# Performance work log

Hardware: AMD Instinct MI355X
Metric: run time of the kernel (lower is better)

Reference implementation:

```python
import jax, jax.numpy as jnp
import numpy as np

N, E, H, D, IN = 50000, 800000, 4, 64, 2  # nodes, edges, heads, head_dim, in_dim
NEG_SLOPE = 0.2  # DGL GATConv default leaky_relu slope


def setup_inputs() -> dict:
    key = jax.random.key(0)
    ks = jax.random.split(key, 16)
    p = lambda k, shape: jax.random.normal(k, shape, jnp.float32) * 0.1
    return dict(
        positions=jax.random.normal(ks[0], (N, IN), jnp.float32),
        src=jax.random.randint(ks[1], (E,), 0, N, jnp.int32),
        dst=jax.random.randint(ks[2], (E,), 0, N, jnp.int32),
        # conv1: in=2 -> 4 heads x 64; residual needs a projection (2 != 256)
        W1=p(ks[3], (IN, H * D)), al1=p(ks[4], (H, D)), ar1=p(ks[5], (H, D)),
        resW1=p(ks[6], (IN, H * D)),
        # conv2/conv3: in=256 == H*D -> identity residual in DGL
        W2=p(ks[7], (H * D, H * D)), al2=p(ks[8], (H, D)), ar2=p(ks[9], (H, D)),
        W3=p(ks[10], (H * D, H * D)), al3=p(ks[11], (H, D)), ar3=p(ks[12], (H, D)),
        # edge-scoring MLP: Linear(64,64)+ReLU, Linear(64,1)+Sigmoid
        mW1=p(ks[13], (D, D)), mb1=jnp.zeros((D,), jnp.float32),
        mW2=p(ks[14], (D, 1)), mb2=jnp.zeros((1,), jnp.float32),
    )


def _gat_layer(h, W, al, ar, src, dst, res, activation):
    """One DGL-style GATConv. h:[N,Fin] -> [N,H,D]. res:[N,H,D] residual."""
    feat = (h @ W).reshape(N, H, D)
    el = (feat * al).sum(-1)                       # [N,H]
    er = (feat * ar).sum(-1)                       # [N,H]
    e = jax.nn.leaky_relu(el[src] + er[dst], NEG_SLOPE)  # [E,H]
    # edge softmax over incoming edges of each dst node
    emax = jax.ops.segment_max(e, dst, num_segments=N)
    emax = jnp.where(jnp.isfinite(emax), emax, 0.0)      # guard empty segments
    ex = jnp.exp(e - emax[dst])
    den = jax.ops.segment_sum(ex, dst, num_segments=N)
    alpha = ex / jnp.maximum(den, 1e-9)[dst]             # [E,H]
    out = jax.ops.segment_sum(feat[src] * alpha[:, :, None], dst, num_segments=N)
    out = out + res
    if activation:
        out = jax.nn.relu(out)
    return out


def reference(positions, W1, al1, ar1, resW1, W2, al2, ar2, W3, al3, ar3,
              mW1, mb1, mW2, mb2, src, dst):
    res1 = (positions @ resW1).reshape(N, H, D)
    h = _gat_layer(positions, W1, al1, ar1, src, dst, res1, True).reshape(N, H * D)
    h = _gat_layer(h, W2, al2, ar2, src, dst, h.reshape(N, H, D), True).reshape(N, H * D)
    h = _gat_layer(h, W3, al3, ar3, src, dst, h.reshape(N, H, D), False).mean(1)  # [N,D]
    x = jnp.abs(h[src] - h[dst])                   # [E,D]
    score = jax.nn.sigmoid(jax.nn.relu(x @ mW1 + mb1) @ mW2 + mb2)
    return score.squeeze(-1)                       # [E]
```

## Files before the change

kernel.cpp:

```cpp
#include <hip/hip_runtime.h>
#include <hip/hip_bf16.h>

#define NN 50000
#define EE 800000

typedef short short8 __attribute__((ext_vector_type(8)));
typedef float f32x4 __attribute__((ext_vector_type(4)));

__device__ __forceinline__ float lrelu(float x) { return x > 0.f ? x : 0.2f * x; }

__device__ __forceinline__ unsigned short f2bf(float x) {
    __hip_bfloat16 b = __float2bfloat16(x);
    return *(unsigned short*)&b;
}
__device__ __forceinline__ float bf2f(unsigned short u) {
    return __uint_as_float(((unsigned int)u) << 16);
}

__global__ void hist_k(const int* __restrict__ dst, int* __restrict__ deg) {
    int i = blockIdx.x * 256 + threadIdx.x;
    if (i < EE) atomicAdd(&deg[dst[i]], 1);
}

__global__ __launch_bounds__(1024) void scan_k(const int* __restrict__ deg,
                                               int* __restrict__ row_ptr,
                                               int* __restrict__ cursor) {
    __shared__ int wsum[16];
    int tid = threadIdx.x, lane = tid & 63, w = tid >> 6;
    int carry = 0;
    for (int base = 0; base < NN; base += 1024) {
        int i = base + tid;
        int v = (i < NN) ? deg[i] : 0;
        int x = v;
#pragma unroll
        for (int off = 1; off < 64; off <<= 1) {
            int y = __shfl_up(x, off);
            if (lane >= off) x += y;
        }
        if (lane == 63) wsum[w] = x;
        __syncthreads();
        if (tid < 16) {
            int s = wsum[tid];
#pragma unroll
            for (int off = 1; off < 16; off <<= 1) {
                int y = __shfl_up(s, off);
                if (tid >= off) s += y;
            }
            wsum[tid] = s;
        }
        __syncthreads();
        int woff = w ? wsum[w - 1] : 0;
        int excl = carry + woff + x - v;
        if (i < NN) { row_ptr[i] = excl; cursor[i] = excl; }
        carry += wsum[15];
        __syncthreads();
    }
    if (tid == 0) row_ptr[NN] = carry;
}

__global__ void scatter_k(const int* __restrict__ src, const int* __restrict__ dst,
                          int* __restrict__ cursor, int* __restrict__ csr_src) {
    int i = blockIdx.x * 256 + threadIdx.x;
    if (i < EE) {
        int slot = atomicAdd(&cursor[dst[i]], 1);
        csr_src[slot] = src[i];
    }
}

__global__ __launch_bounds__(256) void bconv_k(const float* __restrict__ W2,
                                               const float* __restrict__ W3,
                                               const float* __restrict__ mW1,
                                               unsigned short* __restrict__ BT2,
                                               unsigned short* __restrict__ BT3,
                                               unsigned short* __restrict__ W1Tb) {
    int tid = blockIdx.x * 256 + threadIdx.x;
    int k = tid & 255, n = tid >> 8;
    BT2[n * 256 + k] = f2bf(W2[k * 256 + n]);
    BT3[n * 256 + k] = f2bf(W3[k * 256 + n]);
    if (tid < 4096) {
        int kk = tid & 63, nn = tid >> 6;
        W1Tb[nn * 64 + kk] = f2bf(mW1[kk * 64 + nn]);
    }
}

__global__ __launch_bounds__(256) void eler1_k(const float* __restrict__ pos,
                                               const float* __restrict__ W1,
                                               const float* __restrict__ al,
                                               const float* __restrict__ ar,
                                               float* __restrict__ el,
                                               float* __restrict__ er) {
    int wid = blockIdx.x * 4 + (threadIdx.x >> 6);
    int lane = threadIdx.x & 63;
    if (wid >= NN) return;
    int f = lane * 4;
    float4 w0 = *(const float4*)&W1[f];
    float4 w1 = *(const float4*)&W1[256 + f];
    float4 a4 = *(const float4*)&al[f];
    float4 r4 = *(const float4*)&ar[f];
    float2 p = *(const float2*)&pos[wid * 2];
    float fx = p.x * w0.x + p.y * w1.x;
    float fy = p.x * w0.y + p.y * w1.y;
    float fz = p.x * w0.z + p.y * w1.z;
    float fw = p.x * w0.w + p.y * w1.w;
    float pl = fx * a4.x + fy * a4.y + fz * a4.z + fw * a4.w;
    float pr = fx * r4.x + fy * r4.y + fz * r4.z + fw * r4.w;
#pragma unroll
    for (int off = 1; off < 16; off <<= 1) {
        pl += __shfl_xor(pl, off);
        pr += __shfl_xor(pr, off);
    }
    if ((lane & 15) == 0) {
        int h = lane >> 4;
        el[wid * 4 + h] = pl;
        er[wid * 4 + h] = pr;
    }
}

__global__ __launch_bounds__(256) void agg1_k(const float* __restrict__ pos,
                                              const float* __restrict__ W1,
                                              const float* __restrict__ resW1,
                                              const float* __restrict__ el,
                                              const float* __restrict__ er,
                                              const int* __restrict__ row_ptr,
                                              const int* __restrict__ csr_src,
                                              unsigned short* __restrict__ hb16) {
    int wid = blockIdx.x * 4 + (threadIdx.x >> 6);
    int lane = threadIdx.x & 63;
    if (wid >= NN) return;
    int f = lane * 4;
    int start = row_ptr[wid], end = row_ptr[wid + 1];
    int h = lane >> 4;
    float eh = er[wid * 4 + h];

    float ap0 = 0.f, ap1 = 0.f, den = 0.f;
    int s = start;
    for (; s + 3 < end; s += 4) {
        int sn0 = csr_src[s], sn1 = csr_src[s + 1];
        int sn2 = csr_src[s + 2], sn3 = csr_src[s + 3];
        float e0 = el[sn0 * 4 + h], e1 = el[sn1 * 4 + h];
        float e2 = el[sn2 * 4 + h], e3 = el[sn3 * 4 + h];
        float2 p0 = *(const float2*)&pos[sn0 * 2];
        float2 p1 = *(const float2*)&pos[sn1 * 2];
        float2 p2 = *(const float2*)&pos[sn2 * 2];
        float2 p3 = *(const float2*)&pos[sn3 * 2];
        float w0 = __expf(lrelu(e0 + eh)), w1 = __expf(lrelu(e1 + eh));
        float w2 = __expf(lrelu(e2 + eh)), w3 = __expf(lrelu(e3 + eh));
        den += (w0 + w1) + (w2 + w3);
        ap0 += w0 * p0.x + w1 * p1.x + w2 * p2.x + w3 * p3.x;
        ap1 += w0 * p0.y + w1 * p1.y + w2 * p2.y + w3 * p3.y;
    }
    for (; s < end; ++s) {
        int sn = csr_src[s];
        float w = __expf(lrelu(el[sn * 4 + h] + eh));
        float2 p = *(const float2*)&pos[sn * 2];
        den += w;
        ap0 += w * p.x;
        ap1 += w * p.y;
    }
    float inv = 1.f / fmaxf(den, 1e-9f);
    ap0 *= inv;
    ap1 *= inv;

    float4 w0 = *(const float4*)&W1[f];
    float4 w1 = *(const float4*)&W1[256 + f];
    float4 rw0 = *(const float4*)&resW1[f];
    float4 rw1 = *(const float4*)&resW1[256 + f];
    float2 pd = *(const float2*)&pos[wid * 2];
    float4 o;
    o.x = fmaxf(ap0 * w0.x + ap1 * w1.x + pd.x * rw0.x + pd.y * rw1.x, 0.f);
    o.y = fmaxf(ap0 * w0.y + ap1 * w1.y + pd.x * rw0.y + pd.y * rw1.y, 0.f);
    o.z = fmaxf(ap0 * w0.z + ap1 * w1.z + pd.x * rw0.z + pd.y * rw1.z, 0.f);
    o.w = fmaxf(ap0 * w0.w + ap1 * w1.w + pd.x * rw0.w + pd.y * rw1.w, 0.f);
    ushort4 ob;
    ob.x = f2bf(o.x); ob.y = f2bf(o.y); ob.z = f2bf(o.z); ob.w = f2bf(o.w);
    *(ushort4*)&hb16[(size_t)wid * 256 + f] = ob;
}

__global__ __launch_bounds__(256) void agg_k(const unsigned short* __restrict__ featb,
                                             const float* __restrict__ el,
                                             const float* __restrict__ er,
                                             const int* __restrict__ row_ptr,
                                             const int* __restrict__ csr_src,
                                             unsigned short* __restrict__ hb16) {
    int wid = blockIdx.x * 4 + (threadIdx.x >> 6);
    int lane = threadIdx.x & 63;
    if (wid >= NN) return;
    int f = lane * 4;
    int start = row_ptr[wid], end = row_ptr[wid + 1];
    int h = lane >> 4;
    float eh = er[wid * 4 + h];

    float4 acc = {0.f, 0.f, 0.f, 0.f};
    float den = 0.f;
    int s = start;
    for (; s + 3 < end; s += 4) {
        int sn0 = csr_src[s], sn1 = csr_src[s + 1];
        int sn2 = csr_src[s + 2], sn3 = csr_src[s + 3];
        float e0 = el[sn0 * 4 + h], e1 = el[sn1 * 4 + h];
        float e2 = el[sn2 * 4 + h], e3 = el[sn3 * 4 + h];
        ushort4 v0 = *(const ushort4*)&featb[(size_t)sn0 * 256 + f];
        ushort4 v1 = *(const ushort4*)&featb[(size_t)sn1 * 256 + f];
        ushort4 v2 = *(const ushort4*)&featb[(size_t)sn2 * 256 + f];
        ushort4 v3 = *(const ushort4*)&featb[(size_t)sn3 * 256 + f];
        float w0 = __expf(lrelu(e0 + eh)), w1 = __expf(lrelu(e1 + eh));
        float w2 = __expf(lrelu(e2 + eh)), w3 = __expf(lrelu(e3 + eh));
        den += (w0 + w1) + (w2 + w3);
        acc.x += w0 * bf2f(v0.x) + w1 * bf2f(v1.x) + w2 * bf2f(v2.x) + w3 * bf2f(v3.x);
        acc.y += w0 * bf2f(v0.y) + w1 * bf2f(v1.y) + w2 * bf2f(v2.y) + w3 * bf2f(v3.y);
        acc.z += w0 * bf2f(v0.z) + w1 * bf2f(v1.z) + w2 * bf2f(v2.z) + w3 * bf2f(v3.z);
        acc.w += w0 * bf2f(v0.w) + w1 * bf2f(v1.w) + w2 * bf2f(v2.w) + w3 * bf2f(v3.w);
    }
    for (; s < end; ++s) {
        int sn = csr_src[s];
        float w = __expf(lrelu(el[sn * 4 + h] + eh));
        ushort4 v = *(const ushort4*)&featb[(size_t)sn * 256 + f];
        den += w;
        acc.x += w * bf2f(v.x);
        acc.y += w * bf2f(v.y);
        acc.z += w * bf2f(v.z);
        acc.w += w * bf2f(v.w);
    }
    float inv = 1.f / fmaxf(den, 1e-9f);
    ushort4 rb = *(const ushort4*)&hb16[(size_t)wid * 256 + f];
    float4 o;
    o.x = fmaxf(acc.x * inv + bf2f(rb.x), 0.f);
    o.y = fmaxf(acc.y * inv + bf2f(rb.y), 0.f);
    o.z = fmaxf(acc.z * inv + bf2f(rb.z), 0.f);
    o.w = fmaxf(acc.w * inv + bf2f(rb.w), 0.f);
    ushort4 ob;
    ob.x = f2bf(o.x); ob.y = f2bf(o.y); ob.z = f2bf(o.z); ob.w = f2bf(o.w);
    *(ushort4*)&hb16[(size_t)wid * 256 + f] = ob;
}

__global__ __launch_bounds__(256) void agg3_k(const unsigned short* __restrict__ featb,
                                              const float* __restrict__ el,
                                              const float* __restrict__ er,
                                              const int* __restrict__ row_ptr,
                                              const int* __restrict__ csr_src,
                                              const unsigned short* __restrict__ hresb,
                                              unsigned short* __restrict__ hsmallb) {
    int wid = blockIdx.x * 4 + (threadIdx.x >> 6);
    int lane = threadIdx.x & 63;
    if (wid >= NN) return;
    int f = lane * 4;
    int start = row_ptr[wid], end = row_ptr[wid + 1];
    int h = lane >> 4;
    float eh = er[wid * 4 + h];

    float4 acc = {0.f, 0.f, 0.f, 0.f};
    float den = 0.f;
    int s = start;
    for (; s + 3 < end; s += 4) {
        int sn0 = csr_src[s], sn1 = csr_src[s + 1];
        int sn2 = csr_src[s + 2], sn3 = csr_src[s + 3];
        float e0 = el[sn0 * 4 + h], e1 = el[sn1 * 4 + h];
        float e2 = el[sn2 * 4 + h], e3 = el[sn3 * 4 + h];
        ushort4 v0 = *(const ushort4*)&featb[(size_t)sn0 * 256 + f];
        ushort4 v1 = *(const ushort4*)&featb[(size_t)sn1 * 256 + f];
        ushort4 v2 = *(const ushort4*)&featb[(size_t)sn2 * 256 + f];
        ushort4 v3 = *(const ushort4*)&featb[(size_t)sn3 * 256 + f];
        float w0 = __expf(lrelu(e0 + eh)), w1 = __expf(lrelu(e1 + eh));
        float w2 = __expf(lrelu(e2 + eh)), w3 = __expf(lrelu(e3 + eh));
        den += (w0 + w1) + (w2 + w3);
        acc.x += w0 * bf2f(v0.x) + w1 * bf2f(v1.x) + w2 * bf2f(v2.x) + w3 * bf2f(v3.x);
        acc.y += w0 * bf2f(v0.y) + w1 * bf2f(v1.y) + w2 * bf2f(v2.y) + w3 * bf2f(v3.y);
        acc.z += w0 * bf2f(v0.z) + w1 * bf2f(v1.z) + w2 * bf2f(v2.z) + w3 * bf2f(v3.z);
        acc.w += w0 * bf2f(v0.w) + w1 * bf2f(v1.w) + w2 * bf2f(v2.w) + w3 * bf2f(v3.w);
    }
    for (; s < end; ++s) {
        int sn = csr_src[s];
        float w = __expf(lrelu(el[sn * 4 + h] + eh));
        ushort4 v = *(const ushort4*)&featb[(size_t)sn * 256 + f];
        den += w;
        acc.x += w * bf2f(v.x);
        acc.y += w * bf2f(v.y);
        acc.z += w * bf2f(v.z);
        acc.w += w * bf2f(v.w);
    }
    float inv = 1.f / fmaxf(den, 1e-9f);
    ushort4 rb = *(const ushort4*)&hresb[(size_t)wid * 256 + f];
    float4 o;
    o.x = acc.x * inv + bf2f(rb.x);
    o.y = acc.y * inv + bf2f(rb.y);
    o.z = acc.z * inv + bf2f(rb.z);
    o.w = acc.w * inv + bf2f(rb.w);
    o.x += __shfl_xor(o.x, 16); o.y += __shfl_xor(o.y, 16);
    o.z += __shfl_xor(o.z, 16); o.w += __shfl_xor(o.w, 16);
    o.x += __shfl_xor(o.x, 32); o.y += __shfl_xor(o.y, 32);
    o.z += __shfl_xor(o.z, 32); o.w += __shfl_xor(o.w, 32);
    if (lane < 16) {
        ushort4 m4;
        m4.x = f2bf(o.x * 0.25f);
        m4.y = f2bf(o.y * 0.25f);
        m4.z = f2bf(o.z * 0.25f);
        m4.w = f2bf(o.w * 0.25f);
        *(ushort4*)&hsmallb[(size_t)wid * 64 + lane * 4] = m4;
    }
}

__global__ __launch_bounds__(256) void gemm_mfma_k(const unsigned short* __restrict__ Ab,
                                                   const unsigned short* __restrict__ BT,
                                                   const float* __restrict__ al,
                                                   const float* __restrict__ ar,
                                                   unsigned short* __restrict__ C,
                                                   float* __restrict__ el,
                                                   float* __restrict__ er) {
    __shared__ __align__(16) short As[128 * 40];
    __shared__ __align__(16) short Bs[128 * 40];
    int tid = threadIdx.x;
    int lane = tid & 63, wave = tid >> 6;
    int wr = wave >> 1, wc = wave & 1;
    int tileM = blockIdx.x * 128;
    int tileN = blockIdx.y * 128;

    int srow = tid >> 1, sko = (tid & 1) * 16;
    int fm = lane & 15, kg = lane >> 4;

    f32x4 acc[4][4];
#pragma unroll
    for (int i = 0; i < 4; ++i)
#pragma unroll
        for (int j = 0; j < 4; ++j) acc[i][j] = (f32x4){0.f, 0.f, 0.f, 0.f};

    for (int k0 = 0; k0 < 256; k0 += 32) {
        int gr = tileM + srow;
        short8 a0 = (short8)0, a1 = (short8)0;
        if (gr < NN) {
            a0 = *(const short8*)&Ab[(size_t)gr * 256 + k0 + sko];
            a1 = *(const short8*)&Ab[(size_t)gr * 256 + k0 + sko + 8];
        }
        *(short8*)&As[srow * 40 + sko] = a0;
        *(short8*)&As[srow * 40 + sko + 8] = a1;
        short8 b0 = *(const short8*)&BT[(size_t)(tileN + srow) * 256 + k0 + sko];
        short8 b1 = *(const short8*)&BT[(size_t)(tileN + srow) * 256 + k0 + sko + 8];
        *(short8*)&Bs[srow * 40 + sko] = b0;
        *(short8*)&Bs[srow * 40 + sko + 8] = b1;
        __syncthreads();

        short8 afr[4], bfr[4];
#pragma unroll
        for (int mi = 0; mi < 4; ++mi)
            afr[mi] = *(const short8*)&As[(wr * 64 + mi * 16 + fm) * 40 + kg * 8];
#pragma unroll
        for (int ni = 0; ni < 4; ++ni)
            bfr[ni] = *(const short8*)&Bs[(wc * 64 + ni * 16 + fm) * 40 + kg * 8];
#pragma unroll
        for (int mi = 0; mi < 4; ++mi)
#pragma unroll
            for (int ni = 0; ni < 4; ++ni)
                acc[mi][ni] = __builtin_amdgcn_mfma_f32_16x16x32_bf16(
                    afr[mi], bfr[ni], acc[mi][ni], 0, 0, 0);
        __syncthreads();
    }

#pragma unroll
    for (int mi = 0; mi < 4; ++mi) {
#pragma unroll
        for (int ni = 0; ni < 4; ++ni) {
            int col = tileN + wc * 64 + ni * 16 + fm;
#pragma unroll
            for (int r = 0; r < 4; ++r) {
                int row = tileM + wr * 64 + mi * 16 + kg * 4 + r;
                if (row < NN) C[(size_t)row * 256 + col] = f2bf(acc[mi][ni][r]);
            }
        }
    }

    int h = blockIdx.y * 2 + wc;
    float al_r[4], ar_r[4];
#pragma unroll
    for (int ni = 0; ni < 4; ++ni) {
        al_r[ni] = al[h * 64 + ni * 16 + fm];
        ar_r[ni] = ar[h * 64 + ni * 16 + fm];
    }
#pragma unroll
    for (int mi = 0; mi < 4; ++mi) {
#pragma unroll
        for (int r = 0; r < 4; ++r) {
            float tl = acc[mi][0][r] * al_r[0] + acc[mi][1][r] * al_r[1] +
                       acc[mi][2][r] * al_r[2] + acc[mi][3][r] * al_r[3];
            float tr = acc[mi][0][r] * ar_r[0] + acc[mi][1][r] * ar_r[1] +
                       acc[mi][2][r] * ar_r[2] + acc[mi][3][r] * ar_r[3];
#pragma unroll
            for (int off = 1; off < 16; off <<= 1) {
                tl += __shfl_xor(tl, off);
                tr += __shfl_xor(tr, off);
            }
            if (fm == 0) {
                int row = tileM + wr * 64 + mi * 16 + kg * 4 + r;
                if (row < NN) {
                    el[row * 4 + h] = tl;
                    er[row * 4 + h] = tr;
                }
            }
        }
    }
}

__global__ __launch_bounds__(256) void edge_score4_k(const unsigned short* __restrict__ hs,
                                                     const int* __restrict__ src,
                                                     const int* __restrict__ dst,
                                                     const unsigned short* __restrict__ W1Tb,
                                                     const float* __restrict__ mb1,
                                                     const float* __restrict__ mW2,
                                                     const float* __restrict__ mb2,
                                                     float* __restrict__ out) {
    __shared__ __align__(16) unsigned short xs[64 * 72];
    __shared__ __align__(16) unsigned short wt[64 * 72];
    __shared__ float b1s[64], w2s[64];
    int tid = threadIdx.x;
    int e_loc = tid >> 2, q = tid & 3;

    *(short8*)&wt[e_loc * 72 + q * 16]     = *(const short8*)&W1Tb[e_loc * 64 + q * 16];
    *(short8*)&wt[e_loc * 72 + q * 16 + 8] = *(const short8*)&W1Tb[e_loc * 64 + q * 16 + 8];
    if (tid < 64) { b1s[tid] = mb1[tid]; w2s[tid] = mW2[tid]; }

    int e = blockIdx.x * 64 + e_loc;
    int s = src[e], d = dst[e];
    const unsigned short* rs = &hs[(size_t)s * 64 + q * 16];
    const unsigned short* rd = &hs[(size_t)d * 64 + q * 16];
    short8 a0 = *(const short8*)&rs[0];
    short8 a1 = *(const short8*)&rs[8];
    short8 b0 = *(const short8*)&rd[0];
    short8 b1 = *(const short8*)&rd[8];
    short8 x0, x1;
#pragma unroll
    for (int i = 0; i < 8; ++i) {
        x0[i] = (short)f2bf(fabsf(bf2f((unsigned short)a0[i]) - bf2f((unsigned short)b0[i])));
        x1[i] = (short)f2bf(fabsf(bf2f((unsigned short)a1[i]) - bf2f((unsigned short)b1[i])));
    }
    *(short8*)&xs[e_loc * 72 + q * 16]     = x0;
    *(short8*)&xs[e_loc * 72 + q * 16 + 8] = x1;
    __syncthreads();

    int lane = tid & 63, w = tid >> 6;
    int fm = lane & 15, kg = lane >> 4;

    const unsigned short* arow = &xs[(w * 16 + fm) * 72];
    short8 af0 = *(const short8*)&arow[kg * 8];
    short8 af1 = *(const short8*)&arow[32 + kg * 8];

    f32x4 acc[4];
#pragma unroll
    for (int ni = 0; ni < 4; ++ni) acc[ni] = (f32x4){0.f, 0.f, 0.f, 0.f};
#pragma unroll
    for (int ni = 0; ni < 4; ++ni) {
        const unsigned short* brow = &wt[(ni * 16 + fm) * 72];
        short8 bf0 = *(const short8*)&brow[kg * 8];
        short8 bf1 = *(const short8*)&brow[32 + kg * 8];
        acc[ni] = __builtin_amdgcn_mfma_f32_16x16x32_bf16(af0, bf0, acc[ni], 0, 0, 0);
        acc[ni] = __builtin_amdgcn_mfma_f32_16x16x32_bf16(af1, bf1, acc[ni], 0, 0, 0);
    }

    float t0 = 0.f, t1 = 0.f, t2 = 0.f, t3 = 0.f;
#pragma unroll
    for (int ni = 0; ni < 4; ++ni) {
        int n = ni * 16 + fm;
        float bb = b1s[n], ww = w2s[n];
        t0 += fmaxf(acc[ni][0] + bb, 0.f) * ww;
        t1 += fmaxf(acc[ni][1] + bb, 0.f) * ww;
        t2 += fmaxf(acc[ni][2] + bb, 0.f) * ww;
        t3 += fmaxf(acc[ni][3] + bb, 0.f) * ww;
    }
#pragma unroll
    for (int off = 1; off < 16; off <<= 1) {
        t0 += __shfl_xor(t0, off);
        t1 += __shfl_xor(t1, off);
        t2 += __shfl_xor(t2, off);
        t3 += __shfl_xor(t3, off);
    }
    if (fm == 0) {
        float bias = mb2[0];
        int base = blockIdx.x * 64 + w * 16 + kg * 4;
        out[base + 0] = 1.f / (1.f + __expf(-(t0 + bias)));
        out[base + 1] = 1.f / (1.f + __expf(-(t1 + bias)));
        out[base + 2] = 1.f / (1.f + __expf(-(t2 + bias)));
        out[base + 3] = 1.f / (1.f + __expf(-(t3 + bias)));
    }
}

extern "C" void kernel_launch(void* const* d_in, const int* in_sizes, int n_in,
                              void* d_out, int out_size, void* d_ws, size_t ws_size,
                              hipStream_t stream) {
    (void)in_sizes; (void)n_in; (void)out_size; (void)ws_size;
    const float* pos   = (const float*)d_in[0];
    const int*   src   = (const int*)d_in[1];
    const int*   dst   = (const int*)d_in[2];
    const float* W1    = (const float*)d_in[3];
    const float* al1   = (const float*)d_in[4];
    const float* ar1   = (const float*)d_in[5];
    const float* resW1 = (const float*)d_in[6];
    const float* W2    = (const float*)d_in[7];
    const float* al2   = (const float*)d_in[8];
    const float* ar2   = (const float*)d_in[9];
    const float* W3    = (const float*)d_in[10];
    const float* al3   = (const float*)d_in[11];
    const float* ar3   = (const float*)d_in[12];
    const float* mW1   = (const float*)d_in[13];
    const float* mb1   = (const float*)d_in[14];
    const float* mW2   = (const float*)d_in[15];
    const float* mb2   = (const float*)d_in[16];
    float* out = (float*)d_out;

    char* ws = (char*)d_ws;
    size_t off = 0;
    auto alloc = [&](size_t bytes) {
        void* p = ws + off;
        off += (bytes + 255) & ~(size_t)255;
        return p;
    };
    unsigned short* FEATb  = (unsigned short*)alloc((size_t)NN * 256 * 2);
    unsigned short* Hb16   = (unsigned short*)alloc((size_t)NN * 256 * 2);
    unsigned short* BT2    = (unsigned short*)alloc((size_t)256 * 256 * 2);
    unsigned short* BT3    = (unsigned short*)alloc((size_t)256 * 256 * 2);
    unsigned short* W1Tb   = (unsigned short*)alloc((size_t)64 * 64 * 2);
    unsigned short* hsmallb = (unsigned short*)alloc((size_t)NN * 64 * 2);
    float* el     = (float*)alloc((size_t)NN * 4 * 4);
    float* er     = (float*)alloc((size_t)NN * 4 * 4);
    int* deg      = (int*)alloc((size_t)NN * 4);
    int* row_ptr  = (int*)alloc((size_t)(NN + 1) * 4);
    int* cursor   = (int*)alloc((size_t)NN * 4);
    int* csr      = (int*)alloc((size_t)EE * 4);

    hipMemsetAsync(deg, 0, (size_t)NN * 4, stream);
    hist_k<<<(EE + 255) / 256, 256, 0, stream>>>(dst, deg);
    scan_k<<<1, 1024, 0, stream>>>(deg, row_ptr, cursor);
    scatter_k<<<(EE + 255) / 256, 256, 0, stream>>>(src, dst, cursor, csr);
    bconv_k<<<256, 256, 0, stream>>>(W2, W3, mW1, BT2, BT3, W1Tb);

    eler1_k<<<NN / 4 + 1, 256, 0, stream>>>(pos, W1, al1, ar1, el, er);
    agg1_k<<<NN / 4 + 1, 256, 0, stream>>>(pos, W1, resW1, el, er, row_ptr, csr, Hb16);

    dim3 ggrid((NN + 127) / 128, 2);
    gemm_mfma_k<<<ggrid, 256, 0, stream>>>(Hb16, BT2, al2, ar2, FEATb, el, er);
    agg_k<<<NN / 4 + 1, 256, 0, stream>>>(FEATb, el, er, row_ptr, csr, Hb16);

    gemm_mfma_k<<<ggrid, 256, 0, stream>>>(Hb16, BT3, al3, ar3, FEATb, el, er);
    agg3_k<<<NN / 4 + 1, 256, 0, stream>>>(FEATb, el, er, row_ptr, csr, Hb16, hsmallb);

    edge_score4_k<<<EE / 64, 256, 0, stream>>>(hsmallb, src, dst, W1Tb, mb1, mW2, mb2, out);
}
```

Baseline: 494.0 us.

## Parallelize degree scan across blocks and unroll neighbor gathers by eight

Replaces the single-block serial prefix scan over 50000 node degrees with a three-kernel multi-block scan: per-block scan, a scan of block totals, then an offset fix-up. Separately, the edge-aggregation loops in all three GAT layers now issue eight neighbor index, score and feature loads before computing, instead of four. The scan change targets a long one-block serial kernel at the cost of two extra launches. The wider unroll aims to keep more memory requests in flight, at the cost of more registers and a longer scalar tail loop for low-degree nodes.

```diff
diff --git a/kernel.cpp b/kernel.cpp
--- a/kernel.cpp
+++ b/kernel.cpp
@@ -3,6 +3,7 @@
 
 #define NN 50000
 #define EE 800000
+#define NB 196
 
 typedef short short8 __attribute__((ext_vector_type(8)));
 typedef float f32x4 __attribute__((ext_vector_type(4)));
@@ -22,40 +23,64 @@
     if (i < EE) atomicAdd(&deg[dst[i]], 1);
 }
 
-__global__ __launch_bounds__(1024) void scan_k(const int* __restrict__ deg,
+__global__ __launch_bounds__(256) void scanA_k(const int* __restrict__ deg,
+                                               int* __restrict__ cscan,
+                                               int* __restrict__ bsum) {
+    __shared__ int wtot[4];
+    int tid = threadIdx.x, lane = tid & 63, w = tid >> 6;
+    int i = blockIdx.x * 256 + tid;
+    int v = (i < NN) ? deg[i] : 0;
+    int x = v;
+#pragma unroll
+    for (int off = 1; off < 64; off <<= 1) {
+        int y = __shfl_up(x, off);
+        if (lane >= off) x += y;
+    }
+    if (lane == 63) wtot[w] = x;
+    __syncthreads();
+    int prefix = 0;
+#pragma unroll
+    for (int j = 0; j < 4; ++j)
+        if (j < w) prefix += wtot[j];
+    x += prefix;
+    if (i < NN) cscan[i] = x;
+    if (tid == 255) bsum[blockIdx.x] = x;
+}
+
+__global__ __launch_bounds__(256) void scanB_k(const int* __restrict__ bsum,
+                                               int* __restrict__ boff) {
+    __shared__ int wtot[4];
+    int tid = threadIdx.x, lane = tid & 63, w = tid >> 6;
+    int v = (tid < NB) ? bsum[tid] : 0;
+    int x = v;
+#pragma unroll
+    for (int off = 1; off < 64; off <<= 1) {
+        int y = __shfl_up(x, off);
+        if (lane >= off) x += y;
+    }
+    if (lane == 63) wtot[w] = x;
+    __syncthreads();
+    int prefix = 0;
+#pragma unroll
+    for (int j = 0; j < 4; ++j)
+        if (j < w) prefix += wtot[j];
+    x += prefix;
+    if (tid < NB) boff[tid] = x - v;
+    if (tid == NB - 1) boff[NB] = x;
+}
+
+__global__ __launch_bounds__(256) void scanC_k(const int* __restrict__ deg,
+                                               const int* __restrict__ cscan,
+                                               const int* __restrict__ boff,
                                                int* __restrict__ row_ptr,
                                                int* __restrict__ cursor) {
-    __shared__ int wsum[16];
-    int tid = threadIdx.x, lane = tid & 63, w = tid >> 6;
-    int carry = 0;
-    for (int base = 0; base < NN; base += 1024) {
-        int i = base + tid;
-        int v = (i < NN) ? deg[i] : 0;
-        int x = v;
-#pragma unroll
-        for (int off = 1; off < 64; off <<= 1) {
-            int y = __shfl_up(x, off);
-            if (lane >= off) x += y;
-        }
-        if (lane == 63) wsum[w] = x;
-        __syncthreads();
-        if (tid < 16) {
-            int s = wsum[tid];
-#pragma unroll
-            for (int off = 1; off < 16; off <<= 1) {
-                int y = __shfl_up(s, off);
-                if (tid >= off) s += y;
-            }
-            wsum[tid] = s;
-        }
-        __syncthreads();
-        int woff = w ? wsum[w - 1] : 0;
-        int excl = carry + woff + x - v;
-        if (i < NN) { row_ptr[i] = excl; cursor[i] = excl; }
-        carry += wsum[15];
-        __syncthreads();
-    }
-    if (tid == 0) row_ptr[NN] = carry;
+    int i = blockIdx.x * 256 + threadIdx.x;
+    if (i < NN) {
+        int e = boff[i >> 8] + cscan[i] - deg[i];
+        row_ptr[i] = e;
+        cursor[i] = e;
+    }
+    if (i == 0) row_ptr[NN] = boff[NB];
 }
 
 __global__ void scatter_k(const int* __restrict__ src, const int* __restrict__ dst,
@@ -134,20 +159,24 @@
 
     float ap0 = 0.f, ap1 = 0.f, den = 0.f;
     int s = start;
-    for (; s + 3 < end; s += 4) {
-        int sn0 = csr_src[s], sn1 = csr_src[s + 1];
-        int sn2 = csr_src[s + 2], sn3 = csr_src[s + 3];
-        float e0 = el[sn0 * 4 + h], e1 = el[sn1 * 4 + h];
-        float e2 = el[sn2 * 4 + h], e3 = el[sn3 * 4 + h];
-        float2 p0 = *(const float2*)&pos[sn0 * 2];
-        float2 p1 = *(const float2*)&pos[sn1 * 2];
-        float2 p2 = *(const float2*)&pos[sn2 * 2];
-        float2 p3 = *(const float2*)&pos[sn3 * 2];
-        float w0 = __expf(lrelu(e0 + eh)), w1 = __expf(lrelu(e1 + eh));
-        float w2 = __expf(lrelu(e2 + eh)), w3 = __expf(lrelu(e3 + eh));
-        den += (w0 + w1) + (w2 + w3);
-        ap0 += w0 * p0.x + w1 * p1.x + w2 * p2.x + w3 * p3.x;
-        ap1 += w0 * p0.y + w1 * p1.y + w2 * p2.y + w3 * p3.y;
+    for (; s + 7 < end; s += 8) {
+        int sn[8];
+#pragma unroll
+        for (int j = 0; j < 8; ++j) sn[j] = csr_src[s + j];
+        float e[8];
+        float2 p[8];
+#pragma unroll
+        for (int j = 0; j < 8; ++j) {
+            e[j] = el[sn[j] * 4 + h];
+            p[j] = *(const float2*)&pos[sn[j] * 2];
+        }
+#pragma unroll
+        for (int j = 0; j < 8; ++j) {
+            float w = __expf(lrelu(e[j] + eh));
+            den += w;
+            ap0 += w * p[j].x;
+            ap1 += w * p[j].y;
+        }
     }
     for (; s < end; ++s) {
         int sn = csr_src[s];
@@ -193,22 +222,26 @@
     float4 acc = {0.f, 0.f, 0.f, 0.f};
     float den = 0.f;
     int s = start;
-    for (; s + 3 < end; s += 4) {
-        int sn0 = csr_src[s], sn1 = csr_src[s + 1];
-        int sn2 = csr_src[s + 2], sn3 = csr_src[s + 3];
-        float e0 = el[sn0 * 4 + h], e1 = el[sn1 * 4 + h];
-        float e2 = el[sn2 * 4 + h], e3 = el[sn3 * 4 + h];
-        ushort4 v0 = *(const ushort4*)&featb[(size_t)sn0 * 256 + f];
-        ushort4 v1 = *(const ushort4*)&featb[(size_t)sn1 * 256 + f];
-        ushort4 v2 = *(const ushort4*)&featb[(size_t)sn2 * 256 + f];
-        ushort4 v3 = *(const ushort4*)&featb[(size_t)sn3 * 256 + f];
-        float w0 = __expf(lrelu(e0 + eh)), w1 = __expf(lrelu(e1 + eh));
-        float w2 = __expf(lrelu(e2 + eh)), w3 = __expf(lrelu(e3 + eh));
-        den += (w0 + w1) + (w2 + w3);
-        acc.x += w0 * bf2f(v0.x) + w1 * bf2f(v1.x) + w2 * bf2f(v2.x) + w3 * bf2f(v3.x);
-        acc.y += w0 * bf2f(v0.y) + w1 * bf2f(v1.y) + w2 * bf2f(v2.y) + w3 * bf2f(v3.y);
-        acc.z += w0 * bf2f(v0.z) + w1 * bf2f(v1.z) + w2 * bf2f(v2.z) + w3 * bf2f(v3.z);
-        acc.w += w0 * bf2f(v0.w) + w1 * bf2f(v1.w) + w2 * bf2f(v2.w) + w3 * bf2f(v3.w);
+    for (; s + 7 < end; s += 8) {
+        int sn[8];
+#pragma unroll
+        for (int j = 0; j < 8; ++j) sn[j] = csr_src[s + j];
+        float e[8];
+        ushort4 v[8];
+#pragma unroll
+        for (int j = 0; j < 8; ++j) {
+            e[j] = el[sn[j] * 4 + h];
+            v[j] = *(const ushort4*)&featb[(size_t)sn[j] * 256 + f];
+        }
+#pragma unroll
+        for (int j = 0; j < 8; ++j) {
+            float w = __expf(lrelu(e[j] + eh));
+            den += w;
+            acc.x += w * bf2f(v[j].x);
+            acc.y += w * bf2f(v[j].y);
+            acc.z += w * bf2f(v[j].z);
+            acc.w += w * bf2f(v[j].w);
+        }
     }
     for (; s < end; ++s) {
         int sn = csr_src[s];
@@ -250,22 +283,26 @@
     float4 acc = {0.f, 0.f, 0.f, 0.f};
     float den = 0.f;
     int s = start;
-    for (; s + 3 < end; s += 4) {
-        int sn0 = csr_src[s], sn1 = csr_src[s + 1];
-        int sn2 = csr_src[s + 2], sn3 = csr_src[s + 3];
-        float e0 = el[sn0 * 4 + h], e1 = el[sn1 * 4 + h];
-        float e2 = el[sn2 * 4 + h], e3 = el[sn3 * 4 + h];
-        ushort4 v0 = *(const ushort4*)&featb[(size_t)sn0 * 256 + f];
-        ushort4 v1 = *(const ushort4*)&featb[(size_t)sn1 * 256 + f];
-        ushort4 v2 = *(const ushort4*)&featb[(size_t)sn2 * 256 + f];
-        ushort4 v3 = *(const ushort4*)&featb[(size_t)sn3 * 256 + f];
-        float w0 = __expf(lrelu(e0 + eh)), w1 = __expf(lrelu(e1 + eh));
-        float w2 = __expf(lrelu(e2 + eh)), w3 = __expf(lrelu(e3 + eh));
-        den += (w0 + w1) + (w2 + w3);
-        acc.x += w0 * bf2f(v0.x) + w1 * bf2f(v1.x) + w2 * bf2f(v2.x) + w3 * bf2f(v3.x);
-        acc.y += w0 * bf2f(v0.y) + w1 * bf2f(v1.y) + w2 * bf2f(v2.y) + w3 * bf2f(v3.y);
-        acc.z += w0 * bf2f(v0.z) + w1 * bf2f(v1.z) + w2 * bf2f(v2.z) + w3 * bf2f(v3.z);
-        acc.w += w0 * bf2f(v0.w) + w1 * bf2f(v1.w) + w2 * bf2f(v2.w) + w3 * bf2f(v3.w);
+    for (; s + 7 < end; s += 8) {
+        int sn[8];
+#pragma unroll
+        for (int j = 0; j < 8; ++j) sn[j] = csr_src[s + j];
+        float e[8];
+        ushort4 v[8];
+#pragma unroll
+        for (int j = 0; j < 8; ++j) {
+            e[j] = el[sn[j] * 4 + h];
+            v[j] = *(const ushort4*)&featb[(size_t)sn[j] * 256 + f];
+        }
+#pragma unroll
+        for (int j = 0; j < 8; ++j) {
+            float w = __expf(lrelu(e[j] + eh));
+            den += w;
+            acc.x += w * bf2f(v[j].x);
+            acc.y += w * bf2f(v[j].y);
+            acc.z += w * bf2f(v[j].z);
+            acc.w += w * bf2f(v[j].w);
+        }
     }
     for (; s < end; ++s) {
         int sn = csr_src[s];
@@ -518,13 +555,18 @@
     float* el     = (float*)alloc((size_t)NN * 4 * 4);
     float* er     = (float*)alloc((size_t)NN * 4 * 4);
     int* deg      = (int*)alloc((size_t)NN * 4);
+    int* cscan    = (int*)alloc((size_t)NN * 4);
+    int* bsum     = (int*)alloc((size_t)NB * 4);
+    int* boff     = (int*)alloc((size_t)(NB + 1) * 4);
     int* row_ptr  = (int*)alloc((size_t)(NN + 1) * 4);
     int* cursor   = (int*)alloc((size_t)NN * 4);
     int* csr      = (int*)alloc((size_t)EE * 4);
 
     hipMemsetAsync(deg, 0, (size_t)NN * 4, stream);
     hist_k<<<(EE + 255) / 256, 256, 0, stream>>>(dst, deg);
-    scan_k<<<1, 1024, 0, stream>>>(deg, row_ptr, cursor);
+    scanA_k<<<NB, 256, 0, stream>>>(deg, cscan, bsum);
+    scanB_k<<<1, 256, 0, stream>>>(bsum, boff);
+    scanC_k<<<NB, 256, 0, stream>>>(deg, cscan, boff, row_ptr, cursor);
     scatter_k<<<(EE + 255) / 256, 256, 0, stream>>>(src, dst, cursor, csr);
     bconv_k<<<256, 256, 0, stream>>>(W2, W3, mW1, BT2, BT3, W1Tb);
 
```

Measured after the change: 458.3 us. -7.2%, faster.

## Parallelize degree scan and drop LDS staging in GEMM and edge scorer

Applied to the files above, without the earlier changes.

Replaces the single-block serial prefix scan with a three-kernel multi-block scan (block scans, block-offset scan, fixup), removing a long single-workgroup loop. The bf16 MFMA GEMM now loads A/B fragments directly from global memory instead of staging through shared memory with barriers. The edge scorer likewise reads weights and biases directly from global memory instead of copying them to LDS. The changes trade LDS traffic and barriers for possibly less coalesced, repeated global reads, and add two extra kernel launches.

```diff
diff --git a/kernel.cpp b/kernel.cpp
--- a/kernel.cpp
+++ b/kernel.cpp
@@ -3,6 +3,7 @@
 
 #define NN 50000
 #define EE 800000
+#define NB 196
 
 typedef short short8 __attribute__((ext_vector_type(8)));
 typedef float f32x4 __attribute__((ext_vector_type(4)));
@@ -22,40 +23,64 @@
     if (i < EE) atomicAdd(&deg[dst[i]], 1);
 }
 
-__global__ __launch_bounds__(1024) void scan_k(const int* __restrict__ deg,
+__global__ __launch_bounds__(256) void scanA_k(const int* __restrict__ deg,
+                                               int* __restrict__ cscan,
+                                               int* __restrict__ bsum) {
+    __shared__ int wtot[4];
+    int tid = threadIdx.x, lane = tid & 63, w = tid >> 6;
+    int i = blockIdx.x * 256 + tid;
+    int v = (i < NN) ? deg[i] : 0;
+    int x = v;
+#pragma unroll
+    for (int off = 1; off < 64; off <<= 1) {
+        int y = __shfl_up(x, off);
+        if (lane >= off) x += y;
+    }
+    if (lane == 63) wtot[w] = x;
+    __syncthreads();
+    int prefix = 0;
+#pragma unroll
+    for (int j = 0; j < 4; ++j)
+        if (j < w) prefix += wtot[j];
+    x += prefix;
+    if (i < NN) cscan[i] = x;
+    if (tid == 255) bsum[blockIdx.x] = x;
+}
+
+__global__ __launch_bounds__(256) void scanB_k(const int* __restrict__ bsum,
+                                               int* __restrict__ boff) {
+    __shared__ int wtot[4];
+    int tid = threadIdx.x, lane = tid & 63, w = tid >> 6;
+    int v = (tid < NB) ? bsum[tid] : 0;
+    int x = v;
+#pragma unroll
+    for (int off = 1; off < 64; off <<= 1) {
+        int y = __shfl_up(x, off);
+        if (lane >= off) x += y;
+    }
+    if (lane == 63) wtot[w] = x;
+    __syncthreads();
+    int prefix = 0;
+#pragma unroll
+    for (int j = 0; j < 4; ++j)
+        if (j < w) prefix += wtot[j];
+    x += prefix;
+    if (tid < NB) boff[tid] = x - v;
+    if (tid == NB - 1) boff[NB] = x;
+}
+
+__global__ __launch_bounds__(256) void scanC_k(const int* __restrict__ deg,
+                                               const int* __restrict__ cscan,
+                                               const int* __restrict__ boff,
                                                int* __restrict__ row_ptr,
                                                int* __restrict__ cursor) {
-    __shared__ int wsum[16];
-    int tid = threadIdx.x, lane = tid & 63, w = tid >> 6;
-    int carry = 0;
-    for (int base = 0; base < NN; base += 1024) {
-        int i = base + tid;
-        int v = (i < NN) ? deg[i] : 0;
-        int x = v;
-#pragma unroll
-        for (int off = 1; off < 64; off <<= 1) {
-            int y = __shfl_up(x, off);
-            if (lane >= off) x += y;
-        }
-        if (lane == 63) wsum[w] = x;
-        __syncthreads();
-        if (tid < 16) {
-            int s = wsum[tid];
-#pragma unroll
-            for (int off = 1; off < 16; off <<= 1) {
-                int y = __shfl_up(s, off);
-                if (tid >= off) s += y;
-            }
-            wsum[tid] = s;
-        }
-        __syncthreads();
-        int woff = w ? wsum[w - 1] : 0;
-        int excl = carry + woff + x - v;
-        if (i < NN) { row_ptr[i] = excl; cursor[i] = excl; }
-        carry += wsum[15];
-        __syncthreads();
-    }
-    if (tid == 0) row_ptr[NN] = carry;
+    int i = blockIdx.x * 256 + threadIdx.x;
+    if (i < NN) {
+        int e = boff[i >> 8] + cscan[i] - deg[i];
+        row_ptr[i] = e;
+        cursor[i] = e;
+    }
+    if (i == 0) row_ptr[NN] = boff[NB];
 }
 
 __global__ void scatter_k(const int* __restrict__ src, const int* __restrict__ dst,
@@ -305,52 +330,46 @@
                                                    unsigned short* __restrict__ C,
                                                    float* __restrict__ el,
                                                    float* __restrict__ er) {
-    __shared__ __align__(16) short As[128 * 40];
-    __shared__ __align__(16) short Bs[128 * 40];
     int tid = threadIdx.x;
     int lane = tid & 63, wave = tid >> 6;
     int wr = wave >> 1, wc = wave & 1;
     int tileM = blockIdx.x * 128;
     int tileN = blockIdx.y * 128;
-
-    int srow = tid >> 1, sko = (tid & 1) * 16;
     int fm = lane & 15, kg = lane >> 4;
 
+    const unsigned short* arow[4];
+#pragma unroll
+    for (int mi = 0; mi < 4; ++mi) {
+        int r = tileM + wr * 64 + mi * 16 + fm;
+        if (r >= NN) r = NN - 1;
+        arow[mi] = Ab + (size_t)r * 256;
+    }
+    const unsigned short* brow[4];
+#pragma unroll
+    for (int ni = 0; ni < 4; ++ni)
+        brow[ni] = BT + (size_t)(tileN + wc * 64 + ni * 16 + fm) * 256;
+
     f32x4 acc[4][4];
 #pragma unroll
     for (int i = 0; i < 4; ++i)
 #pragma unroll
         for (int j = 0; j < 4; ++j) acc[i][j] = (f32x4){0.f, 0.f, 0.f, 0.f};
 
+#pragma unroll
     for (int k0 = 0; k0 < 256; k0 += 32) {
-        int gr = tileM + srow;
-        short8 a0 = (short8)0, a1 = (short8)0;
-        if (gr < NN) {
-            a0 = *(const short8*)&Ab[(size_t)gr * 256 + k0 + sko];
-            a1 = *(const short8*)&Ab[(size_t)gr * 256 + k0 + sko + 8];
-        }
-        *(short8*)&As[srow * 40 + sko] = a0;
-        *(short8*)&As[srow * 40 + sko + 8] = a1;
-        short8 b0 = *(const short8*)&BT[(size_t)(tileN + srow) * 256 + k0 + sko];
-        short8 b1 = *(const short8*)&BT[(size_t)(tileN + srow) * 256 + k0 + sko + 8];
-        *(short8*)&Bs[srow * 40 + sko] = b0;
-        *(short8*)&Bs[srow * 40 + sko + 8] = b1;
-        __syncthreads();
-
         short8 afr[4], bfr[4];
 #pragma unroll
         for (int mi = 0; mi < 4; ++mi)
-            afr[mi] = *(const short8*)&As[(wr * 64 + mi * 16 + fm) * 40 + kg * 8];
+            afr[mi] = *(const short8*)&arow[mi][k0 + kg * 8];
 #pragma unroll
         for (int ni = 0; ni < 4; ++ni)
-            bfr[ni] = *(const short8*)&Bs[(wc * 64 + ni * 16 + fm) * 40 + kg * 8];
+            bfr[ni] = *(const short8*)&brow[ni][k0 + kg * 8];
 #pragma unroll
         for (int mi = 0; mi < 4; ++mi)
 #pragma unroll
             for (int ni = 0; ni < 4; ++ni)
                 acc[mi][ni] = __builtin_amdgcn_mfma_f32_16x16x32_bf16(
                     afr[mi], bfr[ni], acc[mi][ni], 0, 0, 0);
-        __syncthreads();
     }
 
 #pragma unroll
@@ -406,14 +425,8 @@
                                                      const float* __restrict__ mb2,
                                                      float* __restrict__ out) {
     __shared__ __align__(16) unsigned short xs[64 * 72];
-    __shared__ __align__(16) unsigned short wt[64 * 72];
-    __shared__ float b1s[64], w2s[64];
     int tid = threadIdx.x;
     int e_loc = tid >> 2, q = tid & 3;
-
-    *(short8*)&wt[e_loc * 72 + q * 16]     = *(const short8*)&W1Tb[e_loc * 64 + q * 16];
-    *(short8*)&wt[e_loc * 72 + q * 16 + 8] = *(const short8*)&W1Tb[e_loc * 64 + q * 16 + 8];
-    if (tid < 64) { b1s[tid] = mb1[tid]; w2s[tid] = mW2[tid]; }
 
     int e = blockIdx.x * 64 + e_loc;
     int s = src[e], d = dst[e];
@@ -445,7 +458,7 @@
     for (int ni = 0; ni < 4; ++ni) acc[ni] = (f32x4){0.f, 0.f, 0.f, 0.f};
 #pragma unroll
     for (int ni = 0; ni < 4; ++ni) {
-        const unsigned short* brow = &wt[(ni * 16 + fm) * 72];
+        const unsigned short* brow = &W1Tb[(ni * 16 + fm) * 64];
         short8 bf0 = *(const short8*)&brow[kg * 8];
         short8 bf1 = *(const short8*)&brow[32 + kg * 8];
         acc[ni] = __builtin_amdgcn_mfma_f32_16x16x32_bf16(af0, bf0, acc[ni], 0, 0, 0);
@@ -456,7 +469,7 @@
 #pragma unroll
     for (int ni = 0; ni < 4; ++ni) {
         int n = ni * 16 + fm;
-        float bb = b1s[n], ww = w2s[n];
+        float bb = mb1[n], ww = mW2[n];
         t0 += fmaxf(acc[ni][0] + bb, 0.f) * ww;
         t1 += fmaxf(acc[ni][1] + bb, 0.f) * ww;
         t2 += fmaxf(acc[ni][2] + bb, 0.f) * ww;
@@ -518,13 +531,18 @@
     float* el     = (float*)alloc((size_t)NN * 4 * 4);
     float* er     = (float*)alloc((size_t)NN * 4 * 4);
     int* deg      = (int*)alloc((size_t)NN * 4);
+    int* cscan    = (int*)alloc((size_t)NN * 4);
+    int* bsum     = (int*)alloc((size_t)NB * 4);
+    int* boff     = (int*)alloc((size_t)(NB + 1) * 4);
     int* row_ptr  = (int*)alloc((size_t)(NN + 1) * 4);
     int* cursor   = (int*)alloc((size_t)NN * 4);
     int* csr      = (int*)alloc((size_t)EE * 4);
 
     hipMemsetAsync(deg, 0, (size_t)NN * 4, stream);
     hist_k<<<(EE + 255) / 256, 256, 0, stream>>>(dst, deg);
-    scan_k<<<1, 1024, 0, stream>>>(deg, row_ptr, cursor);
+    scanA_k<<<NB, 256, 0, stream>>>(deg, cscan, bsum);
+    scanB_k<<<1, 256, 0, stream>>>(bsum, boff);
+    scanC_k<<<NB, 256, 0, stream>>>(deg, cscan, boff, row_ptr, cursor);
     scatter_k<<<(EE + 255) / 256, 256, 0, stream>>>(src, dst, cursor, csr);
     bconv_k<<<256, 256, 0, stream>>>(W2, W3, mW1, BT2, BT3, W1Tb);
 
```

After: 515.8 us. 1.04x slower.
